# Performance work log

Hardware: AMD Instinct MI355X
Metric: run time of the kernel (lower is better)

## Reference

```python
import jax, jax.numpy as jnp
import numpy as np

VAR_CXCY = 0.1   # variances[0]
VAR_WH = 0.2     # variances[1]
MIN_OVERLAP = 0.5
NEG_POS_RATIO = 3


def cxcy_to_xyxy(b):
    return jnp.concatenate([b[:, :2] - b[:, 2:] / 2, b[:, :2] + b[:, 2:] / 2], axis=-1)


def jaccard(a, b):
    # a: [O,4] xyxy, b: [P,4] xyxy -> [O,P]
    lt = jnp.maximum(a[:, None, :2], b[None, :, :2])
    rb = jnp.minimum(a[:, None, 2:], b[None, :, 2:])
    wh = jnp.clip(rb - lt, 0.0)
    inter = wh[..., 0] * wh[..., 1]
    area_a = (a[:, 2] - a[:, 0]) * (a[:, 3] - a[:, 1])
    area_b = (b[:, 2] - b[:, 0]) * (b[:, 3] - b[:, 1])
    return inter / (area_a[:, None] + area_b[None, :] - inter)


def xyxy_to_gcxgcy(boxes, priors):
    # boxes: [P,4] xyxy matched per-prior; priors: [P,4] cxcywh
    cxcy = (boxes[:, :2] + boxes[:, 2:]) / 2
    wh = boxes[:, 2:] - boxes[:, :2]
    g_cxcy = (cxcy - priors[:, :2]) / (priors[:, 2:] * VAR_CXCY)
    g_wh = jnp.log(wh / priors[:, 2:]) / VAR_WH
    return jnp.concatenate([g_cxcy, g_wh], axis=-1)


def _match_one(boxes, labels, priors, priors_xyxy):
    # boxes: [O,4] xyxy, labels: [O] int
    overlaps = jaccard(boxes, priors_xyxy)          # [O,P]
    prior_overlaps = overlaps.max(axis=0)            # [P]
    prior_objects = overlaps.argmax(axis=0)          # [P]
    object_priors = overlaps.argmax(axis=1)          # [O] best prior per object
    n_obj = boxes.shape[0]
    prior_objects = prior_objects.at[object_priors].set(jnp.arange(n_obj))
    prior_overlaps = prior_overlaps.at[object_priors].set(1.0)
    lab = labels[prior_objects]
    lab = jnp.where(prior_overlaps < MIN_OVERLAP, 0, lab)
    locs = xyxy_to_gcxgcy(boxes[prior_objects], priors)
    return locs, lab


def setup_inputs() -> dict:
    key = jax.random.key(0)
    B, P, C, O = 64, 8732, 81, 16
    ks = jax.random.split(key, 6)
    predict_locs = jax.random.normal(ks[0], (B, P, 4), dtype=jnp.float32)
    predict_confs = jax.random.normal(ks[1], (B, P, C), dtype=jnp.float32)
    # priors in cxcywh, valid sizes
    p_cxcy = jax.random.uniform(ks[2], (P, 2), minval=0.0, maxval=1.0)
    p_wh = jax.random.uniform(ks[2], (P, 2), minval=0.05, maxval=0.3)
    priors = jnp.concatenate([p_cxcy, p_wh], axis=-1).astype(jnp.float32)
    # targets: valid xyxy boxes in [0,1]
    t_cxcy = jax.random.uniform(ks[3], (B, O, 2), minval=0.2, maxval=0.8)
    t_wh = jax.random.uniform(ks[4], (B, O, 2), minval=0.05, maxval=0.4)
    target_boxes = jnp.concatenate([t_cxcy - t_wh / 2, t_cxcy + t_wh / 2], axis=-1).astype(jnp.float32)
    target_labels = jax.random.randint(ks[5], (B, O), 1, C)
    return {
        'predict_locs': predict_locs,
        'predict_confs': predict_confs,
        'target_boxes': target_boxes,
        'target_labels': target_labels,
        'priors': priors,
    }


def reference(predict_locs, predict_confs, target_boxes, target_labels, priors):
    priors_xyxy = cxcy_to_xyxy(priors)
    true_locs, true_confs = jax.vmap(
        lambda b, l: _match_one(b, l, priors, priors_xyxy)
    )(target_boxes, target_labels)              # [B,P,4], [B,P]

    pos = true_confs != 0                        # [B,P]
    n_pos = pos.sum(axis=1)                      # [B]
    n_pos_total = n_pos.sum().astype(predict_locs.dtype)

    # nn.L1Loss(reduction='mean') over the [n_pos_total, 4] gathered entries
    loc_loss = jnp.sum(jnp.abs(predict_locs - true_locs) * pos[..., None]) / (n_pos_total * 4)

    logp = jax.nn.log_softmax(predict_confs, axis=-1)
    ce = -jnp.take_along_axis(logp, true_confs[..., None], axis=-1)[..., 0]  # [B,P]

    ce_pos_sum = jnp.sum(jnp.where(pos, ce, 0.0))
    ce_neg = jnp.where(pos, 0.0, ce)
    # double-sort rank: rank of each prior when sorted by descending neg loss
    rank = jnp.argsort(jnp.argsort(-ce_neg, axis=1), axis=1)
    hard = rank < (NEG_POS_RATIO * n_pos)[:, None]
    ce_hard_sum = jnp.sum(jnp.where(hard, ce_neg, 0.0))

    conf_loss = (ce_hard_sum + ce_pos_sum) / n_pos_total
    return conf_loss + loc_loss
```

## Files before the change

### kernel.cpp

```cpp
#include <hip/hip_runtime.h>
#include <cstdint>
#include <cstddef>

constexpr int O_C = 16;
constexpr int P_MAX = 8732;
constexpr int CH   = 4;
constexpr int CHP  = 2183;

__device__ __forceinline__ float waveSumF(float v) {
    #pragma unroll
    for (int off = 32; off; off >>= 1) v += __shfl_xor(v, off);
    return v;
}
__device__ __forceinline__ int waveSumI(int v) {
    #pragma unroll
    for (int off = 32; off; off >>= 1) v += __shfl_xor(v, off);
    return v;
}

__global__ void init_okey(unsigned long long* __restrict__ okey, int n) {
    int i = threadIdx.x;
    for (; i < n; i += 256) okey[i] = 0ull;
}

__global__ __launch_bounds__(256) void matchA1(
    const float* __restrict__ target_boxes,
    const float* __restrict__ priors,
    float* __restrict__ ov_out,
    unsigned char* __restrict__ obj_out,
    unsigned long long* __restrict__ okey,
    int P)
{
    const int b    = blockIdx.x / CH;
    const int c    = blockIdx.x % CH;
    const int tid  = threadIdx.x;
    const int lane = tid & 63;
    const int wid  = tid >> 6;

    __shared__ float bx0[O_C], by0[O_C], bx1[O_C], by1[O_C], barea[O_C];
    __shared__ unsigned long long s_wb[O_C * 4];

    if (tid < O_C) {
        const float* tb = target_boxes + ((size_t)b * O_C + tid) * 4;
        float x0 = tb[0], y0 = tb[1], x1 = tb[2], y1 = tb[3];
        bx0[tid] = x0; by0[tid] = y0; bx1[tid] = x1; by1[tid] = y1;
        barea[tid] = (x1 - x0) * (y1 - y0);
    }
    __syncthreads();

    float bi[O_C]; int bp[O_C];
    #pragma unroll
    for (int o = 0; o < O_C; ++o) { bi[o] = -1.0f; bp[o] = 0; }

    const int p0 = c * CHP, p1 = p0 + CHP;
    for (int p = p0 + tid; p < p1; p += 256) {
        float4 pr = reinterpret_cast<const float4*>(priors)[p];
        float px0 = pr.x - pr.z * 0.5f, py0 = pr.y - pr.w * 0.5f;
        float px1 = pr.x + pr.z * 0.5f, py1 = pr.y + pr.w * 0.5f;
        float parea = (px1 - px0) * (py1 - py0);
        float bv = -1.0f; int bo = 0;
        #pragma unroll
        for (int o = 0; o < O_C; ++o) {
            float ix0 = fmaxf(px0, bx0[o]), iy0 = fmaxf(py0, by0[o]);
            float ix1 = fminf(px1, bx1[o]), iy1 = fminf(py1, by1[o]);
            float iw = fmaxf(ix1 - ix0, 0.0f), ih = fmaxf(iy1 - iy0, 0.0f);
            float inter = iw * ih;
            float iou = inter / (barea[o] + parea - inter);
            if (iou > bv) { bv = iou; bo = o; }
            if (iou > bi[o]) { bi[o] = iou; bp[o] = p; }
        }
        ov_out[(size_t)b * P + p]  = bv;
        obj_out[(size_t)b * P + p] = (unsigned char)bo;
    }

    #pragma unroll
    for (int o = 0; o < O_C; ++o) {
        unsigned long long k = (bi[o] >= 0.0f)
            ? (((unsigned long long)__float_as_uint(bi[o]) << 32) |
               (unsigned long long)(0xFFFFFFFFu - (unsigned)bp[o]))
            : 0ull;
        #pragma unroll
        for (int off = 32; off; off >>= 1) {
            unsigned long long k2 = __shfl_xor(k, off);
            if (k2 > k) k = k2;
        }
        if (lane == 0) s_wb[o * 4 + wid] = k;
    }
    __syncthreads();
    if (tid < O_C) {
        unsigned long long k = s_wb[tid * 4];
        #pragma unroll
        for (int w = 1; w < 4; ++w) if (s_wb[tid * 4 + w] > k) k = s_wb[tid * 4 + w];
        if (k) atomicMax(&okey[(size_t)b * O_C + tid], k);
    }
}

__global__ __launch_bounds__(256) void matchA2(
    const float* __restrict__ predict_locs,
    const float* __restrict__ target_boxes,
    const int*   __restrict__ target_labels,
    const float* __restrict__ priors,
    const float* __restrict__ ov_in,
    const unsigned char* __restrict__ obj_in,
    const unsigned long long* __restrict__ okey,
    int*   __restrict__ lab_out,
    int*   __restrict__ npos_p,
    float* __restrict__ loc_p,
    int P)
{
    const int b    = blockIdx.x / CH;
    const int c    = blockIdx.x % CH;
    const int tid  = threadIdx.x;
    const int lane = tid & 63;
    const int wid  = tid >> 6;

    __shared__ float bx0[O_C], by0[O_C], bx1[O_C], by1[O_C];
    __shared__ int   blab[O_C], s_oprior[O_C];
    __shared__ float s_facc[4];
    __shared__ int   s_iacc[4];

    if (tid < O_C) {
        const float* tb = target_boxes + ((size_t)b * O_C + tid) * 4;
        bx0[tid] = tb[0]; by0[tid] = tb[1]; bx1[tid] = tb[2]; by1[tid] = tb[3];
        blab[tid] = target_labels[(size_t)b * O_C + tid];
        unsigned long long k = okey[(size_t)b * O_C + tid];
        s_oprior[tid] = (int)(0xFFFFFFFFu - (unsigned)(k & 0xFFFFFFFFull));
    }
    __syncthreads();

    int   cnt = 0;
    float acc = 0.0f;
    const int p0 = c * CHP, p1 = p0 + CHP;
    for (int p = p0 + tid; p < p1; p += 256) {
        float ov  = ov_in[(size_t)b * P + p];
        int   obj = obj_in[(size_t)b * P + p];
        #pragma unroll
        for (int o = 0; o < O_C; ++o) {
            if (s_oprior[o] == p) { obj = o; ov = 1.0f; }
        }
        int l = (ov < 0.5f) ? 0 : blab[obj];
        lab_out[(size_t)b * P + p] = l;
        if (l != 0) {
            ++cnt;
            float4 pr = reinterpret_cast<const float4*>(priors)[p];
            float x0 = bx0[obj], y0 = by0[obj], x1 = bx1[obj], y1 = by1[obj];
            float cx = (x0 + x1) * 0.5f, cy = (y0 + y1) * 0.5f;
            float w  = x1 - x0,          h  = y1 - y0;
            float g0 = (cx - pr.x) / (pr.z * 0.1f);
            float g1 = (cy - pr.y) / (pr.w * 0.1f);
            float g2 = logf(w / pr.z) / 0.2f;
            float g3 = logf(h / pr.w) / 0.2f;
            float4 pl = reinterpret_cast<const float4*>(predict_locs)[(size_t)b * P + p];
            acc += fabsf(pl.x - g0) + fabsf(pl.y - g1) +
                   fabsf(pl.z - g2) + fabsf(pl.w - g3);
        }
    }
    acc = waveSumF(acc);
    cnt = waveSumI(cnt);
    if (lane == 0) { s_facc[wid] = acc; s_iacc[wid] = cnt; }
    __syncthreads();
    if (tid == 0) {
        npos_p[blockIdx.x] = s_iacc[0] + s_iacc[1] + s_iacc[2] + s_iacc[3];
        loc_p[blockIdx.x]  = s_facc[0] + s_facc[1] + s_facc[2] + s_facc[3];
    }
}

__global__ __launch_bounds__(256) void ce_kernel(
    const float* __restrict__ confs,
    const int*   __restrict__ lab,
    float* __restrict__ ce,
    int rows)
{
    constexpr int C = 81;
    constexpr int R = 64;
    __shared__ float s_x[R * C];

    const int tid  = threadIdx.x;
    const int row0 = blockIdx.x * R;

    {
        const float4* src = reinterpret_cast<const float4*>(confs + (size_t)row0 * C);
        float4* dst = reinterpret_cast<float4*>(s_x);
        const int nv = (R * C) / 4;
        for (int i = tid; i < nv; i += 256) dst[i] = src[i];
    }
    __syncthreads();

    const int rl = tid >> 2;
    const int q  = tid & 3;
    const int s  = q * 20 + (q > 0 ? 1 : 0);
    const int n  = q ? 20 : 21;
    const float* xr = s_x + rl * C;

    float v[21];
    #pragma unroll
    for (int i = 0; i < 21; ++i)
        v[i] = (i < n) ? xr[s + i] : -3.0e38f;

    float m = v[0];
    #pragma unroll
    for (int i = 1; i < 21; ++i) m = fmaxf(m, v[i]);
    m = fmaxf(m, __shfl_xor(m, 1));
    m = fmaxf(m, __shfl_xor(m, 2));

    float sum = 0.0f;
    #pragma unroll
    for (int i = 0; i < 21; ++i)
        if (i < n) sum += __expf(v[i] - m);
    sum += __shfl_xor(sum, 1);
    sum += __shfl_xor(sum, 2);

    const int row = row0 + rl;
    if (q == 0 && row < rows) {
        int l = lab[row];
        ce[row] = m + __logf(sum) - xr[l];
    }
}

__global__ __launch_bounds__(1024) void hard_kernel(
    const float* __restrict__ ce,
    const int*   __restrict__ lab,
    const int*   __restrict__ npos_p,
    float* __restrict__ ce_pos,
    float* __restrict__ ce_hard,
    int P)
{
    const int b    = blockIdx.x;
    const int tid  = threadIdx.x;
    const int lane = tid & 63;
    const int wid  = tid >> 6;

    __shared__ float s_v[P_MAX];
    __shared__ unsigned int hist[16][256];
    __shared__ unsigned int s_sel;
    __shared__ int s_kr;
    __shared__ float s_f[16], s_f2[16];

    const size_t base = (size_t)b * P;
    float possum = 0.0f, negsum = 0.0f;
    for (int p = tid; p < P; p += 1024) {
        float c = ce[base + p];
        int   l = lab[base + p];
        float v;
        if (l != 0) { possum += c; v = 0.0f; }
        else        { negsum += c; v = c; }
        s_v[p] = v;
    }
    possum = waveSumF(possum);
    negsum = waveSumF(negsum);
    if (lane == 0) { s_f[wid] = possum; s_f2[wid] = negsum; }
    __syncthreads();
    float negsum_t = 0.0f, possum_t = 0.0f;
    #pragma unroll
    for (int w = 0; w < 16; ++w) { negsum_t += s_f2[w]; possum_t += s_f[w]; }
    if (tid == 0) ce_pos[b] = possum_t;

    const int K = 3 * (npos_p[b * CH] + npos_p[b * CH + 1] +
                       npos_p[b * CH + 2] + npos_p[b * CH + 3]);
    if (K <= 0) { if (tid == 0) ce_hard[b] = 0.0f; return; }
    if (K >= P) { if (tid == 0) ce_hard[b] = negsum_t; return; }

    unsigned int prefix = 0; int kr = K;
    for (int shift = 24; shift >= 0; shift -= 8) {
        for (int i = tid; i < 16 * 256; i += 1024) (&hist[0][0])[i] = 0;
        __syncthreads();
        unsigned int maskHi = (shift == 24) ? 0u : (0xFFFFFFFFu << (shift + 8));
        for (int p = tid; p < P; p += 1024) {
            unsigned int u = __float_as_uint(s_v[p]);
            if ((u & maskHi) == prefix) atomicAdd(&hist[wid][(u >> shift) & 255], 1u);
        }
        __syncthreads();
        if (wid == 0) {
            unsigned h0 = 0, h1 = 0, h2 = 0, h3 = 0;
            #pragma unroll 4
            for (int w = 0; w < 16; ++w) {
                h0 += hist[w][lane * 4 + 0];
                h1 += hist[w][lane * 4 + 1];
                h2 += hist[w][lane * 4 + 2];
                h3 += hist[w][lane * 4 + 3];
            }
            unsigned own = h0 + h1 + h2 + h3;
            unsigned t = own;
            #pragma unroll
            for (int off = 1; off < 64; off <<= 1) {
                unsigned u = __shfl_down(t, off);
                if (lane + off >= 64) u = 0;
                t += u;
            }
            unsigned Tnext = t - own;
            unsigned cum3 = Tnext;
            unsigned cum2 = cum3 + h3;
            unsigned cum1 = cum2 + h2;
            unsigned cum0 = cum1 + h1;
            unsigned kru = (unsigned)kr;
            int selj = -1; unsigned cg = 0, hs = 0;
            if      (cum3 < kru && kru <= cum3 + h3) { selj = 3; cg = cum3; }
            else if (cum2 < kru && kru <= cum2 + h2) { selj = 2; cg = cum2; }
            else if (cum1 < kru && kru <= cum1 + h1) { selj = 1; cg = cum1; }
            else if (cum0 < kru && kru <= cum0 + h0) { selj = 0; cg = cum0; }
            if (selj >= 0) {
                s_sel = prefix | ((unsigned)(lane * 4 + selj) << shift);
                s_kr  = kr - (int)cg;
            }
        }
        __syncthreads();
        prefix = s_sel; kr = s_kr;
        __syncthreads();
    }

    float sumgt = 0.0f;
    for (int p = tid; p < P; p += 1024) {
        unsigned int u = __float_as_uint(s_v[p]);
        if (u > prefix) sumgt += s_v[p];
    }
    sumgt = waveSumF(sumgt);
    if (lane == 0) s_f[wid] = sumgt;
    __syncthreads();
    if (tid == 0) {
        float sg = 0.0f;
        #pragma unroll
        for (int w = 0; w < 16; ++w) sg += s_f[w];
        ce_hard[b] = sg + (float)kr * __uint_as_float(prefix);
    }
}

__global__ void finalize_kernel(
    const int*   __restrict__ npos_p,
    const float* __restrict__ ce_pos,
    const float* __restrict__ ce_hard,
    const float* __restrict__ loc_p,
    float* __restrict__ out, int B)
{
    const int lane = threadIdx.x;
    int np = 0; float cp = 0.0f, ch = 0.0f, la = 0.0f;
    for (int b = lane; b < B; b += 64) {
        #pragma unroll
        for (int c = 0; c < CH; ++c) {
            np += npos_p[b * CH + c];
            la += loc_p[b * CH + c];
        }
        cp += ce_pos[b]; ch += ce_hard[b];
    }
    #pragma unroll
    for (int off = 32; off; off >>= 1) {
        np += __shfl_xor(np, off);
        cp += __shfl_xor(cp, off);
        ch += __shfl_xor(ch, off);
        la += __shfl_xor(la, off);
    }
    if (lane == 0) {
        float npt = (float)np;
        out[0] = (ch + cp) / npt + la / (npt * 4.0f);
    }
}

extern "C" void kernel_launch(void* const* d_in, const int* in_sizes, int n_in,
                              void* d_out, int out_size, void* d_ws, size_t ws_size,
                              hipStream_t stream) {
    const float* predict_locs  = (const float*)d_in[0];
    const float* predict_confs = (const float*)d_in[1];
    const float* target_boxes  = (const float*)d_in[2];
    const int*   target_labels = (const int*)d_in[3];
    const float* priors        = (const float*)d_in[4];

    const int P = in_sizes[4] / 4;
    const int B = in_sizes[0] / (P * 4);

    char* ws = (char*)d_ws;
    unsigned long long* okey = (unsigned long long*)ws; ws += (size_t)B * O_C * sizeof(unsigned long long);
    int*   lab     = (int*)ws;   ws += (size_t)B * P * sizeof(int);
    float* ce      = (float*)ws; ws += (size_t)B * P * sizeof(float);
    float* ov      = (float*)ws; ws += (size_t)B * P * sizeof(float);
    int*   npos_p  = (int*)ws;   ws += (size_t)B * CH * sizeof(int);
    float* loc_p   = (float*)ws; ws += (size_t)B * CH * sizeof(float);
    float* ce_pos  = (float*)ws; ws += (size_t)B * sizeof(float);
    float* ce_hard = (float*)ws; ws += (size_t)B * sizeof(float);
    unsigned char* obj = (unsigned char*)ws; ws += (size_t)B * P;

    init_okey<<<1, 256, 0, stream>>>(okey, B * O_C);
    matchA1<<<B * CH, 256, 0, stream>>>(target_boxes, priors, ov, obj, okey, P);
    matchA2<<<B * CH, 256, 0, stream>>>(predict_locs, target_boxes, target_labels,
                                        priors, ov, obj, okey, lab, npos_p, loc_p, P);
    const int rows = B * P;
    ce_kernel<<<rows / 64, 256, 0, stream>>>(predict_confs, lab, ce, rows);
    hard_kernel<<<B, 1024, 0, stream>>>(ce, lab, npos_p, ce_pos, ce_hard, P);
    finalize_kernel<<<1, 64, 0, stream>>>(npos_p, ce_pos, ce_hard, loc_p,
                                          (float*)d_out, B);
}
```

Baseline: 86.80 us.

## Fuse label assignment and loc loss into CE kernel, drop atomics and label buffer

Removes the init_okey kernel and the atomicMax by writing per-chunk best-prior keys that consumers reduce. The old matchA2 pass (label assignment plus L1 loc loss) is folded into the cross-entropy kernel, which handles rows that span two batch images. Positive labels are encoded as the sign bit of the stored CE value, so the int label buffer disappears and hard_kernel counts positives itself. The aim is fewer launches and less global traffic, at the cost of more per-row work and a larger loc partial-sum reduction in finalize.

Measured after the change: 89.20 us. 1.03x slower.

```diff
diff --git a/kernel.cpp b/kernel.cpp
--- a/kernel.cpp
+++ b/kernel.cpp
@@ -16,11 +16,6 @@
     #pragma unroll
     for (int off = 32; off; off >>= 1) v += __shfl_xor(v, off);
     return v;
-}
-
-__global__ void init_okey(unsigned long long* __restrict__ okey, int n) {
-    int i = threadIdx.x;
-    for (; i < n; i += 256) okey[i] = 0ull;
 }
 
 __global__ __launch_bounds__(256) void matchA1(
@@ -28,7 +23,7 @@
     const float* __restrict__ priors,
     float* __restrict__ ov_out,
     unsigned char* __restrict__ obj_out,
-    unsigned long long* __restrict__ okey,
+    unsigned long long* __restrict__ okey_part,
     int P)
 {
     const int b    = blockIdx.x / CH;
@@ -52,7 +47,7 @@
     #pragma unroll
     for (int o = 0; o < O_C; ++o) { bi[o] = -1.0f; bp[o] = 0; }
 
-    const int p0 = c * CHP, p1 = p0 + CHP;
+    const int p0 = c * CHP, p1 = min(p0 + CHP, P);
     for (int p = p0 + tid; p < p1; p += 256) {
         float4 pr = reinterpret_cast<const float4*>(priors)[p];
         float px0 = pr.x - pr.z * 0.5f, py0 = pr.y - pr.w * 0.5f;
@@ -91,106 +86,98 @@
         unsigned long long k = s_wb[tid * 4];
         #pragma unroll
         for (int w = 1; w < 4; ++w) if (s_wb[tid * 4 + w] > k) k = s_wb[tid * 4 + w];
-        if (k) atomicMax(&okey[(size_t)b * O_C + tid], k);
-    }
-}
-
-__global__ __launch_bounds__(256) void matchA2(
-    const float* __restrict__ predict_locs,
+        okey_part[(size_t)blockIdx.x * O_C + tid] = k;
+    }
+}
+
+__global__ __launch_bounds__(256) void fused_ce(
+    const float* __restrict__ confs,
+    const float* __restrict__ ov_in,
+    const unsigned char* __restrict__ obj_in,
+    const unsigned long long* __restrict__ okey_part,
     const float* __restrict__ target_boxes,
     const int*   __restrict__ target_labels,
     const float* __restrict__ priors,
-    const float* __restrict__ ov_in,
-    const unsigned char* __restrict__ obj_in,
-    const unsigned long long* __restrict__ okey,
-    int*   __restrict__ lab_out,
-    int*   __restrict__ npos_p,
-    float* __restrict__ loc_p,
-    int P)
+    const float* __restrict__ predict_locs,
+    float* __restrict__ ce_out,
+    float* __restrict__ loc_part,
+    int P, int rows)
 {
-    const int b    = blockIdx.x / CH;
-    const int c    = blockIdx.x % CH;
+    constexpr int C = 81;
+    constexpr int R = 64;
+    __shared__ float s_x[R * C];
+    __shared__ float tbx0[2][O_C], tby0[2][O_C], tbx1[2][O_C], tby1[2][O_C];
+    __shared__ int   tlab[2][O_C], toprior[2][O_C];
+    __shared__ float s_facc[4];
+
     const int tid  = threadIdx.x;
     const int lane = tid & 63;
     const int wid  = tid >> 6;
-
-    __shared__ float bx0[O_C], by0[O_C], bx1[O_C], by1[O_C];
-    __shared__ int   blab[O_C], s_oprior[O_C];
-    __shared__ float s_facc[4];
-    __shared__ int   s_iacc[4];
-
-    if (tid < O_C) {
-        const float* tb = target_boxes + ((size_t)b * O_C + tid) * 4;
-        bx0[tid] = tb[0]; by0[tid] = tb[1]; bx1[tid] = tb[2]; by1[tid] = tb[3];
-        blab[tid] = target_labels[(size_t)b * O_C + tid];
-        unsigned long long k = okey[(size_t)b * O_C + tid];
-        s_oprior[tid] = (int)(0xFFFFFFFFu - (unsigned)(k & 0xFFFFFFFFull));
-    }
-    __syncthreads();
-
-    int   cnt = 0;
-    float acc = 0.0f;
-    const int p0 = c * CHP, p1 = p0 + CHP;
-    for (int p = p0 + tid; p < p1; p += 256) {
-        float ov  = ov_in[(size_t)b * P + p];
-        int   obj = obj_in[(size_t)b * P + p];
+    const int row0 = blockIdx.x * R;
+
+    const int b0     = row0 / P;
+    const int rsplit = min(row0 + R, (b0 + 1) * P);
+    const bool two   = rsplit < row0 + R;
+    const int b1     = two ? b0 + 1 : b0;
+
+    if (tid < 2 * O_C) {
+        const int seg = tid >> 4, o = tid & 15;
+        const int bb  = seg ? b1 : b0;
+        const float* tb = target_boxes + ((size_t)bb * O_C + o) * 4;
+        tbx0[seg][o] = tb[0]; tby0[seg][o] = tb[1];
+        tbx1[seg][o] = tb[2]; tby1[seg][o] = tb[3];
+        tlab[seg][o] = target_labels[(size_t)bb * O_C + o];
+        unsigned long long k = 0ull;
+        #pragma unroll
+        for (int c = 0; c < CH; ++c) {
+            unsigned long long k2 = okey_part[((size_t)bb * CH + c) * O_C + o];
+            if (k2 > k) k = k2;
+        }
+        toprior[seg][o] = (int)(0xFFFFFFFFu - (unsigned)(k & 0xFFFFFFFFull));
+    }
+
+    {
+        const float4* src = reinterpret_cast<const float4*>(confs + (size_t)row0 * C);
+        float4* dst = reinterpret_cast<float4*>(s_x);
+        const int nv = (R * C) / 4;
+        for (int i = tid; i < nv; i += 256) dst[i] = src[i];
+    }
+    __syncthreads();
+
+    const int rl = tid >> 2;
+    const int q  = tid & 3;
+    const int s  = q * 20 + (q > 0 ? 1 : 0);
+    const int n  = q ? 20 : 21;
+    const float* xr = s_x + rl * C;
+    const int row = row0 + rl;
+
+    int   l = 0;
+    float locacc = 0.0f;
+    if (q == 0 && row < rows) {
+        const int seg = (row >= rsplit) ? 1 : 0;
+        const int p   = row - (seg ? b1 : b0) * P;
+        float ov = ov_in[row];
+        int  obj = obj_in[row];
         #pragma unroll
         for (int o = 0; o < O_C; ++o) {
-            if (s_oprior[o] == p) { obj = o; ov = 1.0f; }
-        }
-        int l = (ov < 0.5f) ? 0 : blab[obj];
-        lab_out[(size_t)b * P + p] = l;
+            if (toprior[seg][o] == p) { obj = o; ov = 1.0f; }
+        }
+        l = (ov < 0.5f) ? 0 : tlab[seg][obj];
         if (l != 0) {
-            ++cnt;
             float4 pr = reinterpret_cast<const float4*>(priors)[p];
-            float x0 = bx0[obj], y0 = by0[obj], x1 = bx1[obj], y1 = by1[obj];
+            float x0 = tbx0[seg][obj], y0 = tby0[seg][obj];
+            float x1 = tbx1[seg][obj], y1 = tby1[seg][obj];
             float cx = (x0 + x1) * 0.5f, cy = (y0 + y1) * 0.5f;
             float w  = x1 - x0,          h  = y1 - y0;
             float g0 = (cx - pr.x) / (pr.z * 0.1f);
             float g1 = (cy - pr.y) / (pr.w * 0.1f);
             float g2 = logf(w / pr.z) / 0.2f;
             float g3 = logf(h / pr.w) / 0.2f;
-            float4 pl = reinterpret_cast<const float4*>(predict_locs)[(size_t)b * P + p];
-            acc += fabsf(pl.x - g0) + fabsf(pl.y - g1) +
-                   fabsf(pl.z - g2) + fabsf(pl.w - g3);
-        }
-    }
-    acc = waveSumF(acc);
-    cnt = waveSumI(cnt);
-    if (lane == 0) { s_facc[wid] = acc; s_iacc[wid] = cnt; }
-    __syncthreads();
-    if (tid == 0) {
-        npos_p[blockIdx.x] = s_iacc[0] + s_iacc[1] + s_iacc[2] + s_iacc[3];
-        loc_p[blockIdx.x]  = s_facc[0] + s_facc[1] + s_facc[2] + s_facc[3];
-    }
-}
-
-__global__ __launch_bounds__(256) void ce_kernel(
-    const float* __restrict__ confs,
-    const int*   __restrict__ lab,
-    float* __restrict__ ce,
-    int rows)
-{
-    constexpr int C = 81;
-    constexpr int R = 64;
-    __shared__ float s_x[R * C];
-
-    const int tid  = threadIdx.x;
-    const int row0 = blockIdx.x * R;
-
-    {
-        const float4* src = reinterpret_cast<const float4*>(confs + (size_t)row0 * C);
-        float4* dst = reinterpret_cast<float4*>(s_x);
-        const int nv = (R * C) / 4;
-        for (int i = tid; i < nv; i += 256) dst[i] = src[i];
-    }
-    __syncthreads();
-
-    const int rl = tid >> 2;
-    const int q  = tid & 3;
-    const int s  = q * 20 + (q > 0 ? 1 : 0);
-    const int n  = q ? 20 : 21;
-    const float* xr = s_x + rl * C;
+            float4 pl = reinterpret_cast<const float4*>(predict_locs)[row];
+            locacc = fabsf(pl.x - g0) + fabsf(pl.y - g1) +
+                     fabsf(pl.z - g2) + fabsf(pl.w - g3);
+        }
+    }
 
     float v[21];
     #pragma unroll
@@ -210,17 +197,21 @@
     sum += __shfl_xor(sum, 1);
     sum += __shfl_xor(sum, 2);
 
-    const int row = row0 + rl;
     if (q == 0 && row < rows) {
-        int l = lab[row];
-        ce[row] = m + __logf(sum) - xr[l];
-    }
+        float cev = m + __logf(sum) - xr[l];
+        ce_out[row] = (l != 0) ? -cev : cev;
+    }
+
+    float a = waveSumF(locacc);
+    if (lane == 0) s_facc[wid] = a;
+    __syncthreads();
+    if (tid == 0)
+        loc_part[blockIdx.x] = s_facc[0] + s_facc[1] + s_facc[2] + s_facc[3];
 }
 
 __global__ __launch_bounds__(1024) void hard_kernel(
     const float* __restrict__ ce,
-    const int*   __restrict__ lab,
-    const int*   __restrict__ npos_p,
+    int*   __restrict__ n_pos,
     float* __restrict__ ce_pos,
     float* __restrict__ ce_hard,
     int P)
@@ -235,28 +226,30 @@
     __shared__ unsigned int s_sel;
     __shared__ int s_kr;
     __shared__ float s_f[16], s_f2[16];
+    __shared__ int s_i[16];
 
     const size_t base = (size_t)b * P;
     float possum = 0.0f, negsum = 0.0f;
+    int cnt = 0;
     for (int p = tid; p < P; p += 1024) {
         float c = ce[base + p];
-        int   l = lab[base + p];
-        float v;
-        if (l != 0) { possum += c; v = 0.0f; }
-        else        { negsum += c; v = c; }
-        s_v[p] = v;
+        unsigned u = __float_as_uint(c);
+        float sv;
+        if (u >> 31) { possum += -c; ++cnt; sv = 0.0f; }
+        else         { negsum += c;         sv = c;    }
+        s_v[p] = sv;
     }
     possum = waveSumF(possum);
     negsum = waveSumF(negsum);
-    if (lane == 0) { s_f[wid] = possum; s_f2[wid] = negsum; }
-    __syncthreads();
-    float negsum_t = 0.0f, possum_t = 0.0f;
-    #pragma unroll
-    for (int w = 0; w < 16; ++w) { negsum_t += s_f2[w]; possum_t += s_f[w]; }
-    if (tid == 0) ce_pos[b] = possum_t;
-
-    const int K = 3 * (npos_p[b * CH] + npos_p[b * CH + 1] +
-                       npos_p[b * CH + 2] + npos_p[b * CH + 3]);
+    cnt    = waveSumI(cnt);
+    if (lane == 0) { s_f[wid] = possum; s_f2[wid] = negsum; s_i[wid] = cnt; }
+    __syncthreads();
+    float negsum_t = 0.0f, possum_t = 0.0f; int np = 0;
+    #pragma unroll
+    for (int w = 0; w < 16; ++w) { negsum_t += s_f2[w]; possum_t += s_f[w]; np += s_i[w]; }
+    if (tid == 0) { ce_pos[b] = possum_t; n_pos[b] = np; }
+
+    const int K = 3 * np;
     if (K <= 0) { if (tid == 0) ce_hard[b] = 0.0f; return; }
     if (K >= P) { if (tid == 0) ce_hard[b] = negsum_t; return; }
 
@@ -293,7 +286,7 @@
             unsigned cum1 = cum2 + h2;
             unsigned cum0 = cum1 + h1;
             unsigned kru = (unsigned)kr;
-            int selj = -1; unsigned cg = 0, hs = 0;
+            int selj = -1; unsigned cg = 0;
             if      (cum3 < kru && kru <= cum3 + h3) { selj = 3; cg = cum3; }
             else if (cum2 < kru && kru <= cum2 + h2) { selj = 2; cg = cum2; }
             else if (cum1 < kru && kru <= cum1 + h1) { selj = 1; cg = cum1; }
@@ -324,33 +317,44 @@
     }
 }
 
-__global__ void finalize_kernel(
-    const int*   __restrict__ npos_p,
+__global__ __launch_bounds__(256) void finalize_kernel(
+    const int*   __restrict__ n_pos,
     const float* __restrict__ ce_pos,
     const float* __restrict__ ce_hard,
-    const float* __restrict__ loc_p,
-    float* __restrict__ out, int B)
+    const float* __restrict__ loc_part,
+    float* __restrict__ out, int B, int nblk)
 {
-    const int lane = threadIdx.x;
-    int np = 0; float cp = 0.0f, ch = 0.0f, la = 0.0f;
-    for (int b = lane; b < B; b += 64) {
-        #pragma unroll
-        for (int c = 0; c < CH; ++c) {
-            np += npos_p[b * CH + c];
-            la += loc_p[b * CH + c];
-        }
-        cp += ce_pos[b]; ch += ce_hard[b];
-    }
-    #pragma unroll
-    for (int off = 32; off; off >>= 1) {
-        np += __shfl_xor(np, off);
-        cp += __shfl_xor(cp, off);
-        ch += __shfl_xor(ch, off);
-        la += __shfl_xor(la, off);
-    }
-    if (lane == 0) {
-        float npt = (float)np;
-        out[0] = (ch + cp) / npt + la / (npt * 4.0f);
+    __shared__ float s_f[4];
+    __shared__ float s_res[3];
+    const int tid  = threadIdx.x;
+    const int lane = tid & 63;
+    const int wid  = tid >> 6;
+
+    float la = 0.0f;
+    for (int i = tid; i < nblk; i += 256) la += loc_part[i];
+    la = waveSumF(la);
+    if (lane == 0) s_f[wid] = la;
+
+    if (tid < 64) {
+        int np = 0; float cp = 0.0f, ch = 0.0f;
+        for (int b = lane; b < B; b += 64) {
+            np += n_pos[b]; cp += ce_pos[b]; ch += ce_hard[b];
+        }
+        #pragma unroll
+        for (int off = 32; off; off >>= 1) {
+            np += __shfl_xor(np, off);
+            cp += __shfl_xor(cp, off);
+            ch += __shfl_xor(ch, off);
+        }
+        if (lane == 0) {
+            s_res[0] = (float)np; s_res[1] = cp; s_res[2] = ch;
+        }
+    }
+    __syncthreads();
+    if (tid == 0) {
+        float latot = s_f[0] + s_f[1] + s_f[2] + s_f[3];
+        float npt = s_res[0];
+        out[0] = (s_res[2] + s_res[1]) / npt + latot / (npt * 4.0f);
     }
 }
 
@@ -365,25 +369,25 @@
 
     const int P = in_sizes[4] / 4;
     const int B = in_sizes[0] / (P * 4);
+    const int rows = B * P;
+    const int nblk = (rows + 63) / 64;
 
     char* ws = (char*)d_ws;
-    unsigned long long* okey = (unsigned long long*)ws; ws += (size_t)B * O_C * sizeof(unsigned long long);
-    int*   lab     = (int*)ws;   ws += (size_t)B * P * sizeof(int);
-    float* ce      = (float*)ws; ws += (size_t)B * P * sizeof(float);
-    float* ov      = (float*)ws; ws += (size_t)B * P * sizeof(float);
-    int*   npos_p  = (int*)ws;   ws += (size_t)B * CH * sizeof(int);
-    float* loc_p   = (float*)ws; ws += (size_t)B * CH * sizeof(float);
+    unsigned long long* okey_part = (unsigned long long*)ws;
+    ws += (size_t)B * CH * O_C * sizeof(unsigned long long);
+    float* ce      = (float*)ws; ws += (size_t)rows * sizeof(float);
+    float* ov      = (float*)ws; ws += (size_t)rows * sizeof(float);
+    float* loc_p   = (float*)ws; ws += (size_t)nblk * sizeof(float);
+    int*   n_pos   = (int*)ws;   ws += (size_t)B * sizeof(int);
     float* ce_pos  = (float*)ws; ws += (size_t)B * sizeof(float);
     float* ce_hard = (float*)ws; ws += (size_t)B * sizeof(float);
-    unsigned char* obj = (unsigned char*)ws; ws += (size_t)B * P;
-
-    init_okey<<<1, 256, 0, stream>>>(okey, B * O_C);
-    matchA1<<<B * CH, 256, 0, stream>>>(target_boxes, priors, ov, obj, okey, P);
-    matchA2<<<B * CH, 256, 0, stream>>>(predict_locs, target_boxes, target_labels,
-                                        priors, ov, obj, okey, lab, npos_p, loc_p, P);
-    const int rows = B * P;
-    ce_kernel<<<rows / 64, 256, 0, stream>>>(predict_confs, lab, ce, rows);
-    hard_kernel<<<B, 1024, 0, stream>>>(ce, lab, npos_p, ce_pos, ce_hard, P);
-    finalize_kernel<<<1, 64, 0, stream>>>(npos_p, ce_pos, ce_hard, loc_p,
-                                          (float*)d_out, B);
-}
+    unsigned char* obj = (unsigned char*)ws; ws += (size_t)rows;
+
+    matchA1<<<B * CH, 256, 0, stream>>>(target_boxes, priors, ov, obj, okey_part, P);
+    fused_ce<<<nblk, 256, 0, stream>>>(predict_confs, ov, obj, okey_part,
+                                       target_boxes, target_labels, priors,
+                                       predict_locs, ce, loc_p, P, rows);
+    hard_kernel<<<B, 1024, 0, stream>>>(ce, n_pos, ce_pos, ce_hard, P);
+    finalize_kernel<<<1, 256, 0, stream>>>(n_pos, ce_pos, ce_hard, loc_p,
+                                           (float*)d_out, B, nblk);
+}
```
